# Performance work log

Hardware: AMD Instinct MI355X
Metric: run time of the kernel (lower is better)

The kernel has to match this reference:

```python
import jax, jax.numpy as jnp
import numpy as np

N, E, T, NORB, H, C = 10000, 100000, 200000, 9, 128, 64


def _normalize(v, eps=1e-12):
    # F.normalize: v / max(||v||_2, eps) along last dim
    n = jnp.linalg.norm(v, axis=-1, keepdims=True)
    return v / jnp.maximum(n, eps)


def setup_inputs() -> dict:
    key = jax.random.key(0)
    ks = jax.random.split(key, 24)
    p = lambda i, shape, scale=0.05: jax.random.normal(ks[i], shape, jnp.float32) * scale
    return {
        "x": jax.random.normal(ks[0], (N, H), jnp.float32),
        "cji": jax.random.normal(ks[1], (E, NORB, C), jnp.float32),
        "cutoff_w": jax.random.uniform(ks[2], (E,), jnp.float32),
        "rb": jax.random.normal(ks[3], (E, NORB), jnp.float32),
        "shb": jax.random.normal(ks[4], (T, NORB), jnp.float32),
        "idx_i": jax.random.randint(ks[5], (E,), 0, N),
        "idx_j": jax.random.randint(ks[6], (E,), 0, N),
        "tri_idx_k": jax.random.randint(ks[7], (T,), 0, N),
        "edge_idx_kj": jax.random.randint(ks[8], (T,), 0, E),
        "edge_idx_ji": jax.random.randint(ks[9], (T,), 0, E),
        "w_node": p(10, (H, 2 * C)),
        "b_node": jnp.zeros((2 * C,), jnp.float32),
        "w_c1": p(11, (C, C)),  # coeffs_dim == C here
        "w_c2": p(12, (C, C)),
        "w_t1": p(13, (C, C)),
        "b_t1": jnp.zeros((C,), jnp.float32),
        "w_t2": p(14, (C, C)),
        "b_t2": jnp.zeros((C,), jnp.float32),
        "w_basis": p(15, (C, C)),
        "w_n1": p(16, (2 * C, C)),
        "b_n1": jnp.zeros((C,), jnp.float32),
        "w_n2": p(17, (C, C)),
        "b_n2": jnp.zeros((C,), jnp.float32),
        "w_out": p(18, (C, H)),
    }


def reference(x, cji, cutoff_w, rb, shb, idx_i, idx_j, tri_idx_k, edge_idx_kj,
              edge_idx_ji, w_node, b_node, w_c1, w_c2, w_t1, b_t1, w_t2, b_t2,
              w_basis, w_n1, b_n1, w_n2, b_n2, w_out):
    silu = jax.nn.silu
    x_before = x
    # node_weight -> chunk into (x, xk), each (N, C)
    h = x @ w_node + b_node
    x1, xk = h[:, :C], h[:, C:]
    # f_coeffs: two bias-free Dense + SiLU, per (E, n_orb) position
    cji = silu(silu(cji @ w_c1) @ w_c2)  # (E, NORB, C)
    # cutoff weighting on radial basis
    rb = rb * cutoff_w[:, None]  # (E, NORB)
    # triplet gather + contraction over orbital axis d
    ckj = cji[edge_idx_kj]  # (T, NORB, C)
    three_body_orbs = jnp.einsum("td,tdh->th", rb[edge_idx_kj] * shb, ckj)  # (T, C)
    three_body_orbs = _normalize(three_body_orbs)
    xk_g = jax.nn.sigmoid(xk[tri_idx_k])  # (T, C)
    three_body_w = three_body_orbs * xk_g
    # scatter-sum triplets -> edges, then f_three MLP
    agg = jax.ops.segment_sum(three_body_w, edge_idx_ji, num_segments=E)  # (E, C)
    three_body_w = silu(silu(agg @ w_t1 + b_t1) @ w_t2 + b_t2)  # (E, C)
    cji = cji + cji * three_body_w[:, None, :]  # (E, NORB, C)
    # LCAO weights: contract radial basis with coefficients
    lcao_w = jnp.einsum("ed,edh->eh", rb, cji)  # (E, C)
    lcao_w = _normalize(lcao_w) @ w_basis
    # f_node on gathered endpoint features
    pair = jnp.concatenate([x1[idx_i], x1[idx_j]], axis=-1)  # (E, 2C)
    fnode = silu(silu(pair @ w_n1 + b_n1) @ w_n2 + b_n2)  # (E, C)
    msg = lcao_w * fnode
    out = x_before + jax.ops.segment_sum(msg, idx_i, num_segments=N) @ w_out
    return out
```

## Files before the change

kernel.cpp:

```cpp
#include <hip/hip_runtime.h>
#include <math.h>

typedef __attribute__((ext_vector_type(8))) short bf16x8;
typedef __attribute__((ext_vector_type(4))) float f32x4;
typedef __attribute__((ext_vector_type(4))) unsigned int uint32x4;
typedef unsigned int uint32;
typedef unsigned short ushort;

#define N_NODES 10000
#define E_EDGES 100000
#define T_TRI   200000
#define NORB    9
#define H_DIM   128
#define C_DIM   64
#define LSTR    68

__device__ __forceinline__ ushort f2b_rtne(float f) {
  uint32 u = __float_as_uint(f);
  u += 0x7FFFu + ((u >> 16) & 1u);
  return (ushort)(u >> 16);
}
__device__ __forceinline__ uint32 rtne2(float a, float b) {
  uint32 ua = __float_as_uint(a), ub = __float_as_uint(b);
  ua += 0x7FFFu + ((ua >> 16) & 1u);
  ub += 0x7FFFu + ((ub >> 16) & 1u);
  return (ua >> 16) | (ub & 0xFFFF0000u);
}
__device__ __forceinline__ uint32 trunc2(float a, float b) {
  return (__float_as_uint(a) >> 16) | (__float_as_uint(b) & 0xFFFF0000u);
}
__device__ __forceinline__ float b2f(ushort u) {
  return __uint_as_float(((uint32)u) << 16);
}
__device__ __forceinline__ float blo(uint32 u) {
  return __uint_as_float(u << 16);
}
__device__ __forceinline__ float bhi(uint32 u) {
  return __uint_as_float(u & 0xFFFF0000u);
}
__device__ __forceinline__ float silu_f(float x) {
  return x * __builtin_amdgcn_rcpf(1.0f + __expf(-x));
}
__device__ __forceinline__ float sigmoid_f(float x) {
  return __builtin_amdgcn_rcpf(1.0f + __expf(-x));
}
__device__ __forceinline__ float rl(float v, int k) {
  return __uint_as_float(__builtin_amdgcn_readlane(__float_as_uint(v), k));
}
__device__ __forceinline__ f32x4 mfma16(bf16x8 a, bf16x8 b, f32x4 c) {
  return __builtin_amdgcn_mfma_f32_16x16x32_bf16(a, b, c, 0, 0, 0);
}
#define LDS_FENCE() asm volatile("s_waitcnt lgkmcnt(0)" ::: "memory")

__device__ __forceinline__ bf16x8 pack8(const float* p) {
  f32x4 v0 = *(const f32x4*)p;
  f32x4 v1 = *(const f32x4*)(p + 4);
  uint32x4 u;
  u[0] = trunc2(v0[0], v0[1]);
  u[1] = trunc2(v0[2], v0[3]);
  u[2] = trunc2(v1[0], v1[1]);
  u[3] = trunc2(v1[2], v1[3]);
  return __builtin_bit_cast(bf16x8, u);
}
__device__ __forceinline__ bf16x8 bfrag_w(const float* W, int kt, int ct, int lane) {
  const float* p = W + (size_t)(kt * 32 + ((lane >> 4) * 8)) * 64 + ct * 16 + (lane & 15);
  bf16x8 r;
#pragma unroll
  for (int b = 0; b < 8; ++b) r[b] = (short)f2b_rtne(p[(size_t)b * 64]);
  return r;
}

__global__ __launch_bounds__(128) void k_node_mlp(
    const float* __restrict__ x, const float* __restrict__ w_node,
    const float* __restrict__ b_node, ushort* __restrict__ x1b,
    ushort* __restrict__ sigxkb) {
  __shared__ float xs[H_DIM];
  int n = blockIdx.x;
  int c = threadIdx.x;
  xs[c] = x[(size_t)n * H_DIM + c];
  __syncthreads();
  float acc = b_node[c];
#pragma unroll 8
  for (int k = 0; k < H_DIM; ++k)
    acc = fmaf(xs[k], w_node[k * H_DIM + c], acc);
  if (c < C_DIM)
    x1b[(size_t)n * C_DIM + c] = f2b_rtne(acc);
  else
    sigxkb[(size_t)n * C_DIM + (c - C_DIM)] = f2b_rtne(sigmoid_f(acc));
}

__global__ __launch_bounds__(256) void k_cji_mlp_mfma(
    const float* __restrict__ cji, const float* __restrict__ w_c1,
    const float* __restrict__ w_c2, ushort* __restrict__ cji2) {
  __shared__ __align__(16) float lds_all[4][16 * LSTR];
  int lane = threadIdx.x & 63;
  float* lds = lds_all[threadIdx.x >> 6];
  int wid = (blockIdx.x * 256 + (int)threadIdx.x) >> 6;
  int nw = (gridDim.x * 256) >> 6;
  bf16x8 w1f[2][4], w2f[2][4];
#pragma unroll
  for (int kt = 0; kt < 2; ++kt)
#pragma unroll
    for (int ct = 0; ct < 4; ++ct) {
      w1f[kt][ct] = bfrag_w(w_c1, kt, ct, lane);
      w2f[kt][ct] = bfrag_w(w_c2, kt, ct, lane);
    }
  const int nstrips = (E_EDGES * NORB) / 16;
  int l15 = lane & 15, g = lane >> 4;
  int wrow = g * 4, wcol = l15;
  f32x4 z = {0.f, 0.f, 0.f, 0.f};
  for (int s = wid; s < nstrips; s += nw) {
    const float* ap = cji + (size_t)(s * 16 + l15) * 64 + g * 8;
    bf16x8 a0 = pack8(ap), a1 = pack8(ap + 32);
#pragma unroll
    for (int ct = 0; ct < 4; ++ct) {
      f32x4 acc = mfma16(a0, w1f[0][ct], z);
      acc = mfma16(a1, w1f[1][ct], acc);
#pragma unroll
      for (int r = 0; r < 4; ++r)
        lds[(wrow + r) * LSTR + ct * 16 + wcol] = silu_f(acc[r]);
    }
    LDS_FENCE();
    bf16x8 t0 = pack8(lds + l15 * LSTR + g * 8);
    bf16x8 t1 = pack8(lds + l15 * LSTR + 32 + g * 8);
#pragma unroll
    for (int ct = 0; ct < 4; ++ct) {
      f32x4 acc = mfma16(t0, w2f[0][ct], z);
      acc = mfma16(t1, w2f[1][ct], acc);
#pragma unroll
      for (int r = 0; r < 4; ++r)
        lds[(wrow + r) * LSTR + ct * 16 + wcol] = silu_f(acc[r]);
    }
    LDS_FENCE();
    const float* lp = lds + l15 * LSTR + g * 16;
    f32x4 v0 = *(const f32x4*)lp;
    f32x4 v1 = *(const f32x4*)(lp + 4);
    f32x4 v2 = *(const f32x4*)(lp + 8);
    f32x4 v3 = *(const f32x4*)(lp + 12);
    uint32x4 o0, o1;
    o0[0] = rtne2(v0[0], v0[1]); o0[1] = rtne2(v0[2], v0[3]);
    o0[2] = rtne2(v1[0], v1[1]); o0[3] = rtne2(v1[2], v1[3]);
    o1[0] = rtne2(v2[0], v2[1]); o1[1] = rtne2(v2[2], v2[3]);
    o1[2] = rtne2(v3[0], v3[1]); o1[3] = rtne2(v3[2], v3[3]);
    uint32x4* dst = (uint32x4*)(cji2 + (size_t)(s * 16 + l15) * 64 + g * 16);
    dst[0] = o0;
    dst[1] = o1;
  }
}

__global__ __launch_bounds__(256) void k_triplet2(
    const ushort* __restrict__ cji2, const float* __restrict__ rb,
    const float* __restrict__ cutoff_w, const float* __restrict__ shb,
    const int* __restrict__ tri_idx_k, const int* __restrict__ edge_idx_kj,
    const int* __restrict__ edge_idx_ji, const ushort* __restrict__ sigxkb,
    float* __restrict__ agg) {
  int lane = threadIdx.x & 63;
  int half = lane >> 5;
  int l = lane & 31;
  int wid = (blockIdx.x * 256 + (int)threadIdx.x) >> 6;
  int nw = (gridDim.x * 256) >> 6;
  const uint32* c2 = (const uint32*)cji2;
  const uint32* sx = (const uint32*)sigxkb;
  for (int tb = wid; tb < T_TRI / 2; tb += nw) {
    int t = tb * 2 + half;
    int e = edge_idx_kj[t];
    float cw = cutoff_w[e];
    const uint32* crow = c2 + (size_t)e * (NORB * 32);
    float a0 = 0.f, a1 = 0.f;
#pragma unroll
    for (int d = 0; d < NORB; ++d) {
      uint32 u = crow[d * 32 + l];
      float coeff = rb[e * NORB + d] * cw * shb[t * NORB + d];
      a0 = fmaf(coeff, blo(u), a0);
      a1 = fmaf(coeff, bhi(u), a1);
    }
    float ss = a0 * a0 + a1 * a1;
#pragma unroll
    for (int m = 16; m >= 1; m >>= 1) ss += __shfl_xor(ss, m, 64);
    float scale = __builtin_amdgcn_rsqf(fmaxf(ss, 1e-30f));
    int kn = tri_idx_k[t];
    uint32 gx = sx[(size_t)kn * 32 + l];
    float v0 = a0 * scale * blo(gx);
    float v1 = a1 * scale * bhi(gx);
    int ej = edge_idx_ji[t];
    float* ap = agg + (size_t)ej * C_DIM + 2 * l;
    atomicAdd(ap, v0);
    atomicAdd(ap + 1, v1);
  }
}

__global__ __launch_bounds__(256) void k_tbw_lcao(
    const float* __restrict__ agg, const float* __restrict__ w_t1,
    const float* __restrict__ b_t1, const float* __restrict__ w_t2,
    const float* __restrict__ b_t2, const ushort* __restrict__ cji2,
    const float* __restrict__ rb, const float* __restrict__ cutoff_w,
    const float* __restrict__ w_basis, float* __restrict__ lcao) {
  __shared__ __align__(16) float lds_all[4][16 * LSTR];
  int lane = threadIdx.x & 63;
  float* lds = lds_all[threadIdx.x >> 6];
  int wid = (blockIdx.x * 256 + (int)threadIdx.x) >> 6;
  int nw = (gridDim.x * 256) >> 6;
  bf16x8 wt1[2][4], wt2[2][4], wb[2][4];
  float bt1[4], bt2[4];
  int l15 = lane & 15, g = lane >> 4;
#pragma unroll
  for (int ct = 0; ct < 4; ++ct) {
    bt1[ct] = b_t1[ct * 16 + l15];
    bt2[ct] = b_t2[ct * 16 + l15];
#pragma unroll
    for (int kt = 0; kt < 2; ++kt) {
      wt1[kt][ct] = bfrag_w(w_t1, kt, ct, lane);
      wt2[kt][ct] = bfrag_w(w_t2, kt, ct, lane);
      wb[kt][ct] = bfrag_w(w_basis, kt, ct, lane);
    }
  }
  const int nstrips = E_EDGES / 16;
  int wrow = g * 4, wcol = l15;
  f32x4 z = {0.f, 0.f, 0.f, 0.f};
  for (int s = wid; s < nstrips; s += nw) {
    const float* ap = agg + (size_t)(s * 16 + l15) * 64 + g * 8;
    bf16x8 a0 = pack8(ap), a1 = pack8(ap + 32);
#pragma unroll
    for (int ct = 0; ct < 4; ++ct) {
      f32x4 acc = mfma16(a0, wt1[0][ct], z);
      acc = mfma16(a1, wt1[1][ct], acc);
#pragma unroll
      for (int r = 0; r < 4; ++r)
        lds[(wrow + r) * LSTR + ct * 16 + wcol] = silu_f(acc[r] + bt1[ct]);
    }
    LDS_FENCE();
    bf16x8 t0 = pack8(lds + l15 * LSTR + g * 8);
    bf16x8 t1 = pack8(lds + l15 * LSTR + 32 + g * 8);
    LDS_FENCE();
#pragma unroll
    for (int ct = 0; ct < 4; ++ct) {
      f32x4 acc = mfma16(t0, wt2[0][ct], z);
      acc = mfma16(t1, wt2[1][ct], acc);
#pragma unroll
      for (int r = 0; r < 4; ++r)
        lds[(wrow + r) * LSTR + ct * 16 + wcol] = silu_f(acc[r] + bt2[ct]);
    }
    LDS_FENCE();
    for (int ee = 0; ee < 16; ++ee) {
      int e = s * 16 + ee;
      float cw = cutoff_w[e];
      const ushort* crow = cji2 + (size_t)e * (NORB * C_DIM);
      float acc = 0.f;
#pragma unroll
      for (int d = 0; d < NORB; ++d)
        acc = fmaf(rb[e * NORB + d] * cw, b2f(crow[d * C_DIM + lane]), acc);
      acc *= (1.0f + lds[ee * LSTR + lane]);
      float ss = acc * acc;
#pragma unroll
      for (int m = 32; m >= 1; m >>= 1) ss += __shfl_xor(ss, m, 64);
      float scale = __builtin_amdgcn_rsqf(fmaxf(ss, 1e-30f));
      lds[ee * LSTR + lane] = acc * scale;
    }
    LDS_FENCE();
    bf16x8 n0 = pack8(lds + l15 * LSTR + g * 8);
    bf16x8 n1 = pack8(lds + l15 * LSTR + 32 + g * 8);
    LDS_FENCE();
    f32x4 o[4];
#pragma unroll
    for (int ct = 0; ct < 4; ++ct) {
      o[ct] = mfma16(n0, wb[0][ct], z);
      o[ct] = mfma16(n1, wb[1][ct], o[ct]);
#pragma unroll
      for (int r = 0; r < 4; ++r)
        lds[(wrow + r) * LSTR + ct * 16 + wcol] = o[ct][r];
    }
    LDS_FENCE();
    const float* lp = lds + l15 * LSTR + g * 16;
    f32x4* dst = (f32x4*)(lcao + (size_t)(s * 16 + l15) * 64 + g * 16);
    dst[0] = *(const f32x4*)lp;
    dst[1] = *(const f32x4*)(lp + 4);
    dst[2] = *(const f32x4*)(lp + 8);
    dst[3] = *(const f32x4*)(lp + 12);
  }
}

__global__ __launch_bounds__(256) void k_msg_mfma(
    const ushort* __restrict__ x1b, const int* __restrict__ idx_i,
    const int* __restrict__ idx_j, const float* __restrict__ w_n1,
    const float* __restrict__ b_n1, const float* __restrict__ w_n2,
    const float* __restrict__ b_n2, const float* __restrict__ lcao,
    float* __restrict__ nodeagg) {
  __shared__ __align__(16) float lds_all[4][16 * LSTR];
  int lane = threadIdx.x & 63;
  float* lds = lds_all[threadIdx.x >> 6];
  int wid = (blockIdx.x * 256 + (int)threadIdx.x) >> 6;
  int nw = (gridDim.x * 256) >> 6;
  bf16x8 wn1f[4][4], wn2f[2][4];
  float bn1[4], bn2[4];
  int l15 = lane & 15, g = lane >> 4;
#pragma unroll
  for (int ct = 0; ct < 4; ++ct) {
    bn1[ct] = b_n1[ct * 16 + l15];
    bn2[ct] = b_n2[ct * 16 + l15];
#pragma unroll
    for (int kt = 0; kt < 4; ++kt) wn1f[kt][ct] = bfrag_w(w_n1, kt, ct, lane);
#pragma unroll
    for (int kt = 0; kt < 2; ++kt) wn2f[kt][ct] = bfrag_w(w_n2, kt, ct, lane);
  }
  const int nstrips = E_EDGES / 16;
  int wrow = g * 4, wcol = l15;
  f32x4 z = {0.f, 0.f, 0.f, 0.f};
  for (int s = wid; s < nstrips; s += nw) {
    int er = s * 16 + l15;
    int ii = idx_i[er], jj = idx_j[er];
    const uint32x4* pi = (const uint32x4*)(x1b + (size_t)ii * 64 + g * 8);
    const uint32x4* pj = (const uint32x4*)(x1b + (size_t)jj * 64 + g * 8);
    bf16x8 a0 = __builtin_bit_cast(bf16x8, pi[0]);
    bf16x8 a1 = __builtin_bit_cast(bf16x8, pi[2]);
    bf16x8 a2 = __builtin_bit_cast(bf16x8, pj[0]);
    bf16x8 a3 = __builtin_bit_cast(bf16x8, pj[2]);
#pragma unroll
    for (int ct = 0; ct < 4; ++ct) {
      f32x4 acc = mfma16(a0, wn1f[0][ct], z);
      acc = mfma16(a1, wn1f[1][ct], acc);
      acc = mfma16(a2, wn1f[2][ct], acc);
      acc = mfma16(a3, wn1f[3][ct], acc);
#pragma unroll
      for (int r = 0; r < 4; ++r)
        lds[(wrow + r) * LSTR + ct * 16 + wcol] = silu_f(acc[r] + bn1[ct]);
    }
    LDS_FENCE();
    bf16x8 t0 = pack8(lds + l15 * LSTR + g * 8);
    bf16x8 t1 = pack8(lds + l15 * LSTR + 32 + g * 8);
    f32x4 acc2[4];
#pragma unroll
    for (int ct = 0; ct < 4; ++ct) {
      acc2[ct] = mfma16(t0, wn2f[0][ct], z);
      acc2[ct] = mfma16(t1, wn2f[1][ct], acc2[ct]);
    }
#pragma unroll
    for (int r = 0; r < 4; ++r) {
      int ge = s * 16 + wrow + r;
      int ni = idx_i[ge];
#pragma unroll
      for (int ct = 0; ct < 4; ++ct) {
        float f = silu_f(acc2[ct][r] + bn2[ct]);
        float m = lcao[(size_t)ge * 64 + ct * 16 + l15] * f;
        atomicAdd(&nodeagg[(size_t)ni * 64 + ct * 16 + l15], m);
      }
    }
  }
}

__global__ __launch_bounds__(256) void k_out(
    const float* __restrict__ x, const float* __restrict__ nodeagg,
    const float* __restrict__ w_out, float* __restrict__ out) {
  int lane = threadIdx.x & 63;
  int wid = (blockIdx.x * 256 + (int)threadIdx.x) >> 6;
  int nw = (gridDim.x * 256) >> 6;
  float wo0[64], wo1[64];
#pragma unroll
  for (int k = 0; k < 64; ++k) wo0[k] = w_out[k * H_DIM + lane];
#pragma unroll
  for (int k = 0; k < 64; ++k) wo1[k] = w_out[k * H_DIM + 64 + lane];
  for (int n = wid; n < N_NODES; n += nw) {
    float v = nodeagg[(size_t)n * 64 + lane];
    float a0 = 0.f, a1 = 0.f;
#pragma unroll
    for (int k = 0; k < 64; ++k) {
      float a = rl(v, k);
      a0 = fmaf(a, wo0[k], a0);
      a1 = fmaf(a, wo1[k], a1);
    }
    out[(size_t)n * H_DIM + lane] = x[(size_t)n * H_DIM + lane] + a0;
    out[(size_t)n * H_DIM + 64 + lane] = x[(size_t)n * H_DIM + 64 + lane] + a1;
  }
}

extern "C" void kernel_launch(void* const* d_in, const int* in_sizes, int n_in,
                              void* d_out, int out_size, void* d_ws, size_t ws_size,
                              hipStream_t stream) {
  const float* x         = (const float*)d_in[0];
  const float* cji       = (const float*)d_in[1];
  const float* cutoff_w  = (const float*)d_in[2];
  const float* rb        = (const float*)d_in[3];
  const float* shb       = (const float*)d_in[4];
  const int*   idx_i     = (const int*)d_in[5];
  const int*   idx_j     = (const int*)d_in[6];
  const int*   tri_idx_k = (const int*)d_in[7];
  const int*   e_kj      = (const int*)d_in[8];
  const int*   e_ji      = (const int*)d_in[9];
  const float* w_node    = (const float*)d_in[10];
  const float* b_node    = (const float*)d_in[11];
  const float* w_c1      = (const float*)d_in[12];
  const float* w_c2      = (const float*)d_in[13];
  const float* w_t1      = (const float*)d_in[14];
  const float* b_t1      = (const float*)d_in[15];
  const float* w_t2      = (const float*)d_in[16];
  const float* b_t2      = (const float*)d_in[17];
  const float* w_basis   = (const float*)d_in[18];
  const float* w_n1      = (const float*)d_in[19];
  const float* b_n1      = (const float*)d_in[20];
  const float* w_n2      = (const float*)d_in[21];
  const float* b_n2      = (const float*)d_in[22];
  const float* w_out     = (const float*)d_in[23];
  float* out = (float*)d_out;

  char* ws = (char*)d_ws;
  ushort* x1b    = (ushort*)(ws + 0);
  ushort* sigxkb = (ushort*)(ws + 1280000);
  ushort* cji2   = (ushort*)(ws + 2560000);
  float*  aggbuf = (float*)(ws + 117760000);
  float*  lcao   = (float*)(ws + 143360000);
  float*  nodeagg= (float*)(ws + 168960000);

  hipMemsetAsync(aggbuf, 0, (size_t)6400000 * sizeof(float), stream);
  hipMemsetAsync(nodeagg, 0, (size_t)640000 * sizeof(float), stream);

  k_node_mlp<<<N_NODES, 128, 0, stream>>>(x, w_node, b_node, x1b, sigxkb);
  k_cji_mlp_mfma<<<2048, 256, 0, stream>>>(cji, w_c1, w_c2, cji2);
  k_triplet2<<<2048, 256, 0, stream>>>(cji2, rb, cutoff_w, shb, tri_idx_k, e_kj,
                                       e_ji, sigxkb, aggbuf);
  k_tbw_lcao<<<1024, 256, 0, stream>>>(aggbuf, w_t1, b_t1, w_t2, b_t2, cji2,
                                       rb, cutoff_w, w_basis, lcao);
  k_msg_mfma<<<1024, 256, 0, stream>>>(x1b, idx_i, idx_j, w_n1, b_n1, w_n2,
                                       b_n2, lcao, nodeagg);
  k_out<<<256, 256, 0, stream>>>(x, nodeagg, w_out, out);
}
```

Baseline: 309.4 us.

## Accumulate triplet scatter in bf16 packed atomics and prefetch cji strips

```diff
diff --git a/kernel.cpp b/kernel.cpp
--- a/kernel.cpp
+++ b/kernel.cpp
@@ -50,11 +50,23 @@
 __device__ __forceinline__ f32x4 mfma16(bf16x8 a, bf16x8 b, f32x4 c) {
   return __builtin_amdgcn_mfma_f32_16x16x32_bf16(a, b, c, 0, 0, 0);
 }
+__device__ __forceinline__ void atom_pk_bf16(ushort* addr, uint32 val) {
+  asm volatile("global_atomic_pk_add_bf16 %0, %1, off"
+               :: "v"(addr), "v"(val) : "memory");
+}
 #define LDS_FENCE() asm volatile("s_waitcnt lgkmcnt(0)" ::: "memory")
 
 __device__ __forceinline__ bf16x8 pack8(const float* p) {
   f32x4 v0 = *(const f32x4*)p;
   f32x4 v1 = *(const f32x4*)(p + 4);
+  uint32x4 u;
+  u[0] = trunc2(v0[0], v0[1]);
+  u[1] = trunc2(v0[2], v0[3]);
+  u[2] = trunc2(v1[0], v1[1]);
+  u[3] = trunc2(v1[2], v1[3]);
+  return __builtin_bit_cast(bf16x8, u);
+}
+__device__ __forceinline__ bf16x8 pack8v(f32x4 v0, f32x4 v1) {
   uint32x4 u;
   u[0] = trunc2(v0[0], v0[1]);
   u[1] = trunc2(v0[2], v0[3]);
@@ -109,9 +121,26 @@
   int l15 = lane & 15, g = lane >> 4;
   int wrow = g * 4, wcol = l15;
   f32x4 z = {0.f, 0.f, 0.f, 0.f};
-  for (int s = wid; s < nstrips; s += nw) {
+  int s = wid;
+  f32x4 nv0, nv1, nv2, nv3;
+  if (s < nstrips) {
     const float* ap = cji + (size_t)(s * 16 + l15) * 64 + g * 8;
-    bf16x8 a0 = pack8(ap), a1 = pack8(ap + 32);
+    nv0 = *(const f32x4*)ap;
+    nv1 = *(const f32x4*)(ap + 4);
+    nv2 = *(const f32x4*)(ap + 32);
+    nv3 = *(const f32x4*)(ap + 36);
+  }
+  while (s < nstrips) {
+    f32x4 c0 = nv0, c1 = nv1, c2 = nv2, c3 = nv3;
+    int sn = s + nw;
+    if (sn < nstrips) {
+      const float* np = cji + (size_t)(sn * 16 + l15) * 64 + g * 8;
+      nv0 = *(const f32x4*)np;
+      nv1 = *(const f32x4*)(np + 4);
+      nv2 = *(const f32x4*)(np + 32);
+      nv3 = *(const f32x4*)(np + 36);
+    }
+    bf16x8 a0 = pack8v(c0, c1), a1 = pack8v(c2, c3);
 #pragma unroll
     for (int ct = 0; ct < 4; ++ct) {
       f32x4 acc = mfma16(a0, w1f[0][ct], z);
@@ -145,15 +174,16 @@
     uint32x4* dst = (uint32x4*)(cji2 + (size_t)(s * 16 + l15) * 64 + g * 16);
     dst[0] = o0;
     dst[1] = o1;
-  }
-}
-
-__global__ __launch_bounds__(256) void k_triplet2(
+    s = sn;
+  }
+}
+
+__global__ __launch_bounds__(256) void k_triplet_pk(
     const ushort* __restrict__ cji2, const float* __restrict__ rb,
     const float* __restrict__ cutoff_w, const float* __restrict__ shb,
     const int* __restrict__ tri_idx_k, const int* __restrict__ edge_idx_kj,
     const int* __restrict__ edge_idx_ji, const ushort* __restrict__ sigxkb,
-    float* __restrict__ agg) {
+    ushort* __restrict__ aggb) {
   int lane = threadIdx.x & 63;
   int half = lane >> 5;
   int l = lane & 31;
@@ -183,14 +213,12 @@
     float v0 = a0 * scale * blo(gx);
     float v1 = a1 * scale * bhi(gx);
     int ej = edge_idx_ji[t];
-    float* ap = agg + (size_t)ej * C_DIM + 2 * l;
-    atomicAdd(ap, v0);
-    atomicAdd(ap + 1, v1);
+    atom_pk_bf16(aggb + (size_t)ej * C_DIM + 2 * l, rtne2(v0, v1));
   }
 }
 
 __global__ __launch_bounds__(256) void k_tbw_lcao(
-    const float* __restrict__ agg, const float* __restrict__ w_t1,
+    const ushort* __restrict__ aggb, const float* __restrict__ w_t1,
     const float* __restrict__ b_t1, const float* __restrict__ w_t2,
     const float* __restrict__ b_t2, const ushort* __restrict__ cji2,
     const float* __restrict__ rb, const float* __restrict__ cutoff_w,
@@ -218,8 +246,9 @@
   int wrow = g * 4, wcol = l15;
   f32x4 z = {0.f, 0.f, 0.f, 0.f};
   for (int s = wid; s < nstrips; s += nw) {
-    const float* ap = agg + (size_t)(s * 16 + l15) * 64 + g * 8;
-    bf16x8 a0 = pack8(ap), a1 = pack8(ap + 32);
+    const uint32x4* ap = (const uint32x4*)(aggb + (size_t)(s * 16 + l15) * 64 + g * 8);
+    bf16x8 a0 = __builtin_bit_cast(bf16x8, ap[0]);
+    bf16x8 a1 = __builtin_bit_cast(bf16x8, ap[2]);
 #pragma unroll
     for (int ct = 0; ct < 4; ++ct) {
       f32x4 acc = mfma16(a0, wt1[0][ct], z);
@@ -405,18 +434,18 @@
   ushort* x1b    = (ushort*)(ws + 0);
   ushort* sigxkb = (ushort*)(ws + 1280000);
   ushort* cji2   = (ushort*)(ws + 2560000);
-  float*  aggbuf = (float*)(ws + 117760000);
+  ushort* aggb   = (ushort*)(ws + 117760000);
   float*  lcao   = (float*)(ws + 143360000);
   float*  nodeagg= (float*)(ws + 168960000);
 
-  hipMemsetAsync(aggbuf, 0, (size_t)6400000 * sizeof(float), stream);
-  hipMemsetAsync(nodeagg, 0, (size_t)640000 * sizeof(float), stream);
+  (void)hipMemsetAsync(aggb, 0, (size_t)6400000 * sizeof(ushort), stream);
+  (void)hipMemsetAsync(nodeagg, 0, (size_t)640000 * sizeof(float), stream);
 
   k_node_mlp<<<N_NODES, 128, 0, stream>>>(x, w_node, b_node, x1b, sigxkb);
   k_cji_mlp_mfma<<<2048, 256, 0, stream>>>(cji, w_c1, w_c2, cji2);
-  k_triplet2<<<2048, 256, 0, stream>>>(cji2, rb, cutoff_w, shb, tri_idx_k, e_kj,
-                                       e_ji, sigxkb, aggbuf);
-  k_tbw_lcao<<<1024, 256, 0, stream>>>(aggbuf, w_t1, b_t1, w_t2, b_t2, cji2,
+  k_triplet_pk<<<2048, 256, 0, stream>>>(cji2, rb, cutoff_w, shb, tri_idx_k,
+                                         e_kj, e_ji, sigxkb, aggb);
+  k_tbw_lcao<<<1024, 256, 0, stream>>>(aggb, w_t1, b_t1, w_t2, b_t2, cji2,
                                        rb, cutoff_w, w_basis, lcao);
   k_msg_mfma<<<1024, 256, 0, stream>>>(x1b, idx_i, idx_j, w_n1, b_n1, w_n2,
                                        b_n2, lcao, nodeagg);
```

Result: faster. 257.6 us (-16.7%).
